# Performance work log

Hardware: AMD Instinct MI355X
Metric: run time of the kernel (lower is better)

Reference implementation:

```python
import jax, jax.numpy as jnp
import numpy as np

B, T, I, H, L, O = 256, 256, 512, 1024, 2, 5


def setup_inputs() -> dict:
    key = jax.random.key(0)
    ks = jax.random.split(key, 8)
    x = jax.random.normal(ks[0], (B, T, I), dtype=jnp.float32)
    hidden = jnp.zeros((L, 2, B, H), dtype=jnp.float32)  # [layer, (h,c), B, H]
    # per-layer stacked gate weights: [4(gates f,i,g,o), H, in+H]
    W0 = jax.random.normal(ks[1], (4, H, I + H), dtype=jnp.float32) * 0.01
    b0 = jnp.zeros((4, H), dtype=jnp.float32)
    W1 = jax.random.normal(ks[2], (4, H, H + H), dtype=jnp.float32) * 0.01
    b1 = jnp.zeros((4, H), dtype=jnp.float32)
    W_out = jax.random.normal(ks[3], (O, H), dtype=jnp.float32) * 0.01
    b_out = jnp.zeros((O,), dtype=jnp.float32)
    return {"x": x, "hidden": hidden, "W0": W0, "b0": b0,
            "W1": W1, "b1": b1, "W_out": W_out, "b_out": b_out}


def _lstm_cell(W, b):
    # W: [4, H, in+H], gates in order (f, i, g, o) matching the torch module
    def cell(carry, x_t):
        h, c = carry
        combined = jnp.concatenate([h, x_t], axis=1)        # [B, H+in]
        gates = jnp.einsum('bk,ghk->gbh', combined, W) + b[:, None, :]
        f = jax.nn.sigmoid(gates[0])
        i = jax.nn.sigmoid(gates[1])
        g = jnp.tanh(gates[2])
        o = jax.nn.sigmoid(gates[3])
        c_new = f * c + i * g
        h_new = o * jnp.tanh(c_new)
        return (h_new, c_new), h_new
    return cell


def reference(x, hidden, W0, b0, W1, b1, W_out, b_out):
    xs = jnp.swapaxes(x, 0, 1)  # [T, B, I]
    finals = []
    for layer, (W, b) in enumerate([(W0, b0), (W1, b1)]):
        h0, c0 = hidden[layer, 0], hidden[layer, 1]
        (hT, cT), ys = jax.lax.scan(_lstm_cell(W, b), (h0, c0), xs)
        xs = ys                      # feed this layer's h sequence to next layer
        finals.append(jnp.stack([hT, cT]))
    last_hidden = xs[-1]             # [B, H], last timestep of top layer
    output = last_hidden @ W_out.T + b_out
    return output, jnp.stack(finals)  # ([B,O], [L,2,B,H])
```

## Files before the change

### kernel.cpp

```cpp
#include <hip/hip_runtime.h>
#include <hip/hip_bf16.h>
#include <cstdint>
#include <cstddef>

#define Bdim 256
#define Tdim 256
#define Idim 512
#define Hdim 1024
#define Odim 5
#define BH (Bdim * Hdim)

using short8 = __attribute__((ext_vector_type(8))) short;
using f32x4  = __attribute__((ext_vector_type(4))) float;
typedef unsigned long long u64;

__device__ __forceinline__ short bf16_of(float f) {
  unsigned u = __builtin_bit_cast(unsigned, f);
  u += 0x7fffu + ((u >> 16) & 1u);
  return (short)(u >> 16);
}

__device__ __forceinline__ float sigmf(float x) {
  return 1.0f / (1.0f + __expf(-x));
}

__global__ __launch_bounds__(256) void k_init(const float* __restrict__ hidden,
    short* __restrict__ h0s0, short* __restrict__ h1s0) {
  int i = blockIdx.x * 256 + threadIdx.x;
  if (i < BH) {
    h0s0[i] = bf16_of(hidden[i]);
    h1s0[i] = bf16_of(hidden[2 * BH + i]);
  }
}

__device__ __forceinline__ void bar_arrive(unsigned* slots, unsigned val) {
  __syncthreads();
  if (threadIdx.x == 0)
    __hip_atomic_store(&slots[blockIdx.x], val, __ATOMIC_RELAXED,
                       __HIP_MEMORY_SCOPE_AGENT);
}

__device__ __forceinline__ void bar_poll(unsigned* slots, unsigned val) {
  if (threadIdx.x < 64) {
    unsigned* p = slots + threadIdx.x * 4;
    for (;;) {
      unsigned v0 = __hip_atomic_load(p + 0, __ATOMIC_RELAXED, __HIP_MEMORY_SCOPE_AGENT);
      unsigned v1 = __hip_atomic_load(p + 1, __ATOMIC_RELAXED, __HIP_MEMORY_SCOPE_AGENT);
      unsigned v2 = __hip_atomic_load(p + 2, __ATOMIC_RELAXED, __HIP_MEMORY_SCOPE_AGENT);
      unsigned v3 = __hip_atomic_load(p + 3, __ATOMIC_RELAXED, __HIP_MEMORY_SCOPE_AGENT);
      bool ok = (v0 >= val) & (v1 >= val) & (v2 >= val) & (v3 >= val);
      if (__all(ok)) break;
      __builtin_amdgcn_s_sleep(1);
    }
  }
}

#define GEMM_H(A0P, A1P, K0, NBLK)                                             \
  for (int blk = 0; blk < (NBLK); ++blk) {                                     \
    short8 Ar0[8], Ar1[8], Br0[8], Br1[8];                                     \
    const int kb = (K0) + blk * 256 + kl;                                      \
    _Pragma("unroll")                                                          \
    for (int u = 0; u < 8; ++u) {                                              \
      const int k = kb + u * 32;                                               \
      Ar0[u] = *(const short8*)((A0P) + k);                                    \
      Ar1[u] = *(const short8*)((A1P) + k);                                    \
      Br0[u] = *(const short8*)(lb0 + k);                                      \
      Br1[u] = *(const short8*)(lb1 + k);                                      \
    }                                                                          \
    _Pragma("unroll")                                                          \
    for (int u = 0; u < 8; ++u) {                                              \
      acc[0][0] = __builtin_amdgcn_mfma_f32_16x16x32_bf16(Ar0[u], Br0[u], acc[0][0], 0, 0, 0); \
      acc[1][0] = __builtin_amdgcn_mfma_f32_16x16x32_bf16(Ar1[u], Br0[u], acc[1][0], 0, 0, 0); \
      acc[0][1] = __builtin_amdgcn_mfma_f32_16x16x32_bf16(Ar0[u], Br1[u], acc[0][1], 0, 0, 0); \
      acc[1][1] = __builtin_amdgcn_mfma_f32_16x16x32_bf16(Ar1[u], Br1[u], acc[1][1], 0, 0, 0); \
    }                                                                          \
  }

#define GEMM_X(XF0, XF1)                                                       \
  for (int blk = 0; blk < 4; ++blk) {                                          \
    f32x4 U0[4][2], U1[4][2]; short8 Bx0[4], Bx1[4];                           \
    const int kb = Hdim + blk * 128 + kl;                                      \
    _Pragma("unroll")                                                          \
    for (int u = 0; u < 4; ++u) {                                              \
      const int k = kb + u * 32;                                               \
      U0[u][0] = *(const f32x4*)((XF0) + k);                                   \
      U0[u][1] = *(const f32x4*)((XF0) + k + 4);                               \
      U1[u][0] = *(const f32x4*)((XF1) + k);                                   \
      U1[u][1] = *(const f32x4*)((XF1) + k + 4);                               \
      Bx0[u] = *(const short8*)(lb0 + k);                                      \
      Bx1[u] = *(const short8*)(lb1 + k);                                      \
    }                                                                          \
    _Pragma("unroll")                                                          \
    for (int u = 0; u < 4; ++u) {                                              \
      short8 a0 = {bf16_of(U0[u][0][0]), bf16_of(U0[u][0][1]), bf16_of(U0[u][0][2]), bf16_of(U0[u][0][3]), \
                   bf16_of(U0[u][1][0]), bf16_of(U0[u][1][1]), bf16_of(U0[u][1][2]), bf16_of(U0[u][1][3])}; \
      short8 a1 = {bf16_of(U1[u][0][0]), bf16_of(U1[u][0][1]), bf16_of(U1[u][0][2]), bf16_of(U1[u][0][3]), \
                   bf16_of(U1[u][1][0]), bf16_of(U1[u][1][1]), bf16_of(U1[u][1][2]), bf16_of(U1[u][1][3])}; \
      acc[0][0] = __builtin_amdgcn_mfma_f32_16x16x32_bf16(a0, Bx0[u], acc[0][0], 0, 0, 0); \
      acc[1][0] = __builtin_amdgcn_mfma_f32_16x16x32_bf16(a1, Bx0[u], acc[1][0], 0, 0, 0); \
      acc[0][1] = __builtin_amdgcn_mfma_f32_16x16x32_bf16(a0, Bx1[u], acc[0][1], 0, 0, 0); \
      acc[1][1] = __builtin_amdgcn_mfma_f32_16x16x32_bf16(a1, Bx1[u], acc[1][1], 0, 0, 0); \
    }                                                                          \
  }

__global__ __launch_bounds__(512, 1) void k_persist(
    const float* __restrict__ W0, const float* __restrict__ b0v,
    const float* __restrict__ W1, const float* __restrict__ b1v,
    const float* __restrict__ hidden,
    const float* __restrict__ x,
    short* __restrict__ h0seq,
    short* __restrict__ h1seq,
    float* __restrict__ finals,
    unsigned* __restrict__ slots, int D) {
  extern __shared__ short lw[];
  const int tid  = threadIdx.x;
  const int wg   = blockIdx.x;
  const bool isL0 = (wg < 128);
  const int slot  = isL0 ? wg : wg - 128;
  const int hcol0 = slot * 8;
  const int K     = isL0 ? (Hdim + Idim) : (2 * Hdim);
  const int pitch = K + 8;
  const int layer = isL0 ? 0 : 1;
  const float* Wsrc = isL0 ? W0 : W1;
  const float* bsrc = isL0 ? b0v : b1v;

  for (int r = 0; r < 32; ++r) {
    const float* src = Wsrc + (size_t)((r >> 3) * Hdim + hcol0 + (r & 7)) * K;
    short* dst = lw + r * pitch;
    for (int k = tid; k < K; k += 512) dst[k] = bf16_of(src[k]);
  }

  const int lane = tid & 63;
  const int wv   = tid >> 6;
  const int col  = lane & 15;
  const int rg   = lane >> 4;
  const int kl   = rg * 8;
  const int row0 = wv * 32 + col;

  float biasv[2];
  #pragma unroll
  for (int n = 0; n < 2; ++n)
    biasv[n] = bsrc[(n * 2 + (col >= 8 ? 1 : 0)) * Hdim + hcol0 + (col & 7)];

  float creg[2][4], hfin[2][4];
  #pragma unroll
  for (int m = 0; m < 2; ++m)
    #pragma unroll
    for (int j = 0; j < 4; ++j) {
      int b = wv * 32 + m * 16 + rg * 4 + j;
      creg[m][j] = hidden[(layer * 2 + 1) * BH + b * Hdim + hcol0 + (col & 7)];
      hfin[m][j] = 0.f;
    }

  if (tid == 0)
    (void)__hip_atomic_load(slots, __ATOMIC_ACQUIRE, __HIP_MEMORY_SCOPE_AGENT);
  __syncthreads();

  const short* lb0 = lw + col * pitch;
  const short* lb1 = lw + (16 + col) * pitch;

  int i_cur = 0, i_prev = 0;
  for (int r = 0; r <= 256; ++r) {
    const bool active = isL0 ? (r < 256) : (r >= 1);
    const int t = isL0 ? r : r - 1;
    const int i_next = (i_cur + 1 == D) ? 0 : i_cur + 1;
    f32x4 acc[2][2] = {};

    if (active && isL0) {
      const float* xf0 = x + (size_t)(row0 * Tdim + t) * Idim - Hdim;
      const float* xf1 = x + (size_t)((row0 + 16) * Tdim + t) * Idim - Hdim;
      GEMM_X(xf0, xf1)
    }
    __builtin_amdgcn_sched_barrier(0);
    if (r > 0) {
      bar_poll(slots, (unsigned)r);
      if (tid == 0 && i_cur == 0)
        (void)__hip_atomic_load(slots, __ATOMIC_ACQUIRE, __HIP_MEMORY_SCOPE_AGENT);
      __syncthreads();
    }

    if (active) {
      const short* Ah = (isL0 ? h0seq + (size_t)i_cur * BH
                               : h1seq + (size_t)i_prev * BH) + row0 * Hdim;
      GEMM_H(Ah, Ah + 16 * Hdim, 0, 4)
      if (!isL0) {
        const short* Ax = h0seq + (size_t)i_cur * BH + row0 * Hdim - Hdim;
        GEMM_H(Ax, Ax + 16 * Hdim, Hdim, 4)
      }
      short* hout = isL0 ? h0seq + (size_t)i_next * BH
                         : h1seq + (size_t)i_cur * BH;
      #pragma unroll
      for (int m = 0; m < 2; ++m) {
        #pragma unroll
        for (int j = 0; j < 4; ++j) {
          float fi  = acc[m][0][j] + biasv[0];
          float go  = acc[m][1][j] + biasv[1];
          float iv_ = __shfl_xor(fi, 8, 64);
          float ov_ = __shfl_xor(go, 8, 64);
          float fv = sigmf(fi), iv = sigmf(iv_);
          float gv = tanhf(go), ov = sigmf(ov_);
          float cn = fv * creg[m][j] + iv * gv;
          creg[m][j] = cn;
          float hn = ov * tanhf(cn);
          hfin[m][j] = hn;
          unsigned hv = (unsigned)(unsigned short)bf16_of(hn);
          unsigned p1 = hv | ((unsigned)__shfl_xor((int)hv, 1, 64) << 16);
          u64 p2 = (u64)p1 | ((u64)(unsigned)__shfl_xor((int)p1, 2, 64) << 32);
          if ((col & 3) == 0 && col < 8) {
            int b = wv * 32 + m * 16 + rg * 4 + j;
            __hip_atomic_store((u64*)(hout + b * Hdim + hcol0 + col), p2,
                               __ATOMIC_RELAXED, __HIP_MEMORY_SCOPE_AGENT);
          }
        }
      }
    }
    if (r < 256) bar_arrive(slots, (unsigned)(r + 1));
    i_prev = i_cur; i_cur = i_next;
  }

  if (col < 8) {
    #pragma unroll
    for (int m = 0; m < 2; ++m)
      #pragma unroll
      for (int j = 0; j < 4; ++j) {
        int b = wv * 32 + m * 16 + rg * 4 + j;
        finals[(layer * 2 + 0) * BH + b * Hdim + hcol0 + col] = hfin[m][j];
        finals[(layer * 2 + 1) * BH + b * Hdim + hcol0 + col] = creg[m][j];
      }
  }
}

__global__ __launch_bounds__(256) void k_outproj(const float* __restrict__ h1f,
    const float* __restrict__ Wout, const float* __restrict__ bout,
    float* __restrict__ out) {
  int b = blockIdx.x;
  int tid = threadIdx.x;
  float hv[4];
  #pragma unroll
  for (int j = 0; j < 4; ++j) hv[j] = h1f[b * Hdim + tid + j * 256];
  __shared__ float red[Odim][4];
  #pragma unroll
  for (int o = 0; o < Odim; ++o) {
    float p = 0.f;
    #pragma unroll
    for (int j = 0; j < 4; ++j) p += hv[j] * Wout[o * Hdim + tid + j * 256];
    #pragma unroll
    for (int s = 32; s > 0; s >>= 1) p += __shfl_down(p, s, 64);
    if ((tid & 63) == 0) red[o][tid >> 6] = p;
  }
  __syncthreads();
  if (tid < Odim)
    out[b * Odim + tid] = red[tid][0] + red[tid][1] + red[tid][2] + red[tid][3] + bout[tid];
}

extern "C" void kernel_launch(void* const* d_in, const int* in_sizes, int n_in,
                              void* d_out, int out_size, void* d_ws, size_t ws_size,
                              hipStream_t stream) {
  const float* x      = (const float*)d_in[0];
  const float* hidden = (const float*)d_in[1];
  const float* W0     = (const float*)d_in[2];
  const float* b0     = (const float*)d_in[3];
  const float* W1     = (const float*)d_in[4];
  const float* b1     = (const float*)d_in[5];
  const float* Wout   = (const float*)d_in[6];
  const float* bout   = (const float*)d_in[7];
  float* out = (float*)d_out;
  float* finals = out + Bdim * Odim;

  char* ws = (char*)d_ws;
  size_t off = 0;
  auto alloc = [&](size_t bytes) {
    void* p = ws + off;
    off += (bytes + 255) & ~(size_t)255;
    return p;
  };
  unsigned* slots = (unsigned*)alloc(256 * sizeof(unsigned));
  const size_t seqSlotBytes = (size_t)BH * 2;
  size_t avail = (ws_size > off) ? (ws_size - off - 512) : 0;
  int D = (int)(avail / (2 * seqSlotBytes));
  if (D > 257) D = 257;
  if (D < 2) D = 2;
  short* h0seq = (short*)alloc((size_t)D * seqSlotBytes);
  short* h1seq = (short*)alloc((size_t)D * seqSlotBytes);

  k_init<<<BH / 256, 256, 0, stream>>>(hidden, h0seq, h1seq);
  hipMemsetAsync(slots, 0, 256 * sizeof(unsigned), stream);

  const int ldsBytes = 32 * (2 * Hdim + 8) * 2;
  hipFuncSetAttribute((const void*)k_persist,
                      hipFuncAttributeMaxDynamicSharedMemorySize, ldsBytes);
  void* args[] = {(void*)&W0, (void*)&b0, (void*)&W1, (void*)&b1,
                  (void*)&hidden, (void*)&x,
                  (void*)&h0seq, (void*)&h1seq,
                  (void*)&finals, (void*)&slots, (void*)&D};
  hipLaunchCooperativeKernel((const void*)k_persist, dim3(256), dim3(512),
                             args, ldsBytes, stream);

  k_outproj<<<Bdim, 256, 0, stream>>>(finals + 2 * BH, Wout, bout, out);
}
```

Before: 8.661 ms.

## Replace global per-step barrier with per-layer counters and decoupled layer pipelining

Swaps the all-256-workgroup slot barrier for 16 padded atomic counters, eight per layer, that workgroups increment. Layer 0 now waits only on its own layer's step count, plus a bounded-lead check against layer 1 so ring buffer slots are not overwritten. Layer 1 waits on layer 0's step r+1 and its own step r, so the two layers can drift apart instead of running in lockstep. The intent is to cut barrier polling cost and let the two layers overlap more freely. In exchange the minimum ring depth rises to 8 and there is more contention from atomic adds on shared counters.

```diff
diff --git a/kernel.cpp b/kernel.cpp
--- a/kernel.cpp
+++ b/kernel.cpp
@@ -33,22 +33,25 @@
   }
 }
 
-__device__ __forceinline__ void bar_arrive(unsigned* slots, unsigned val) {
+__device__ __forceinline__ void ctr_arrive(unsigned* ctr, int c) {
+  __builtin_amdgcn_sched_barrier(0);
   __syncthreads();
   if (threadIdx.x == 0)
-    __hip_atomic_store(&slots[blockIdx.x], val, __ATOMIC_RELAXED,
-                       __HIP_MEMORY_SCOPE_AGENT);
-}
-
-__device__ __forceinline__ void bar_poll(unsigned* slots, unsigned val) {
+    __hip_atomic_fetch_add(&ctr[c * 32], 1u, __ATOMIC_RELAXED,
+                           __HIP_MEMORY_SCOPE_AGENT);
+}
+
+__device__ __forceinline__ void ctr_poll2(unsigned* ctr, unsigned tg0, unsigned tg1) {
   if (threadIdx.x < 64) {
-    unsigned* p = slots + threadIdx.x * 4;
+    const int lane = threadIdx.x;
+    const unsigned tgt = (lane < 8) ? tg0 : (lane < 16 ? tg1 : 0u);
+    unsigned* p = ctr + (lane < 16 ? lane : 0) * 32;
     for (;;) {
-      unsigned v0 = __hip_atomic_load(p + 0, __ATOMIC_RELAXED, __HIP_MEMORY_SCOPE_AGENT);
-      unsigned v1 = __hip_atomic_load(p + 1, __ATOMIC_RELAXED, __HIP_MEMORY_SCOPE_AGENT);
-      unsigned v2 = __hip_atomic_load(p + 2, __ATOMIC_RELAXED, __HIP_MEMORY_SCOPE_AGENT);
-      unsigned v3 = __hip_atomic_load(p + 3, __ATOMIC_RELAXED, __HIP_MEMORY_SCOPE_AGENT);
-      bool ok = (v0 >= val) & (v1 >= val) & (v2 >= val) & (v3 >= val);
+      bool ok = true;
+      if (tgt) {
+        unsigned v = __hip_atomic_load(p, __ATOMIC_RELAXED, __HIP_MEMORY_SCOPE_AGENT);
+        ok = (v >= tgt);
+      }
       if (__all(ok)) break;
       __builtin_amdgcn_s_sleep(1);
     }
@@ -111,7 +114,7 @@
     short* __restrict__ h0seq,
     short* __restrict__ h1seq,
     float* __restrict__ finals,
-    unsigned* __restrict__ slots, int D) {
+    unsigned* __restrict__ ctr, int D) {
   extern __shared__ short lw[];
   const int tid  = threadIdx.x;
   const int wg   = blockIdx.x;
@@ -121,6 +124,8 @@
   const int K     = isL0 ? (Hdim + Idim) : (2 * Hdim);
   const int pitch = K + 8;
   const int layer = isL0 ? 0 : 1;
+  const int myc   = layer * 8 + (wg & 7);
+  const int lead  = D - 4;
   const float* Wsrc = isL0 ? W0 : W1;
   const float* bsrc = isL0 ? b0v : b1v;
 
@@ -153,69 +158,69 @@
     }
 
   if (tid == 0)
-    (void)__hip_atomic_load(slots, __ATOMIC_ACQUIRE, __HIP_MEMORY_SCOPE_AGENT);
+    (void)__hip_atomic_load(ctr, __ATOMIC_ACQUIRE, __HIP_MEMORY_SCOPE_AGENT);
   __syncthreads();
 
   const short* lb0 = lw + col * pitch;
   const short* lb1 = lw + (16 + col) * pitch;
 
-  int i_cur = 0, i_prev = 0;
-  for (int r = 0; r <= 256; ++r) {
-    const bool active = isL0 ? (r < 256) : (r >= 1);
-    const int t = isL0 ? r : r - 1;
+  int i_cur = 0;
+  for (int r = 0; r < 256; ++r) {
     const int i_next = (i_cur + 1 == D) ? 0 : i_cur + 1;
     f32x4 acc[2][2] = {};
-
-    if (active && isL0) {
-      const float* xf0 = x + (size_t)(row0 * Tdim + t) * Idim - Hdim;
-      const float* xf1 = x + (size_t)((row0 + 16) * Tdim + t) * Idim - Hdim;
+    short* hout;
+
+    if (isL0) {
+      const float* xf0 = x + (size_t)(row0 * Tdim + r) * Idim - Hdim;
+      const float* xf1 = x + (size_t)((row0 + 16) * Tdim + r) * Idim - Hdim;
       GEMM_X(xf0, xf1)
+      __builtin_amdgcn_sched_barrier(0);
+      unsigned tg1 = (r > lead) ? 16u * (unsigned)(r - lead) : 0u;
+      if (r > 0 || tg1) ctr_poll2(ctr, 16u * (unsigned)r, tg1);
+      if (tid == 0 && D < 257 && r >= D - 1)
+        (void)__hip_atomic_load(ctr, __ATOMIC_ACQUIRE, __HIP_MEMORY_SCOPE_AGENT);
+      __syncthreads();
+      const short* Ah = h0seq + (size_t)i_cur * BH + row0 * Hdim;
+      GEMM_H(Ah, Ah + 16 * Hdim, 0, 4)
+      hout = h0seq + (size_t)i_next * BH;
+    } else {
+      ctr_poll2(ctr, 16u * (unsigned)(r + 1), 16u * (unsigned)r);
+      if (tid == 0 && D < 257 && r >= D - 1)
+        (void)__hip_atomic_load(ctr, __ATOMIC_ACQUIRE, __HIP_MEMORY_SCOPE_AGENT);
+      __syncthreads();
+      const short* Ax = h0seq + (size_t)i_next * BH + row0 * Hdim - Hdim;
+      GEMM_H(Ax, Ax + 16 * Hdim, Hdim, 4)
+      const short* Ah = h1seq + (size_t)i_cur * BH + row0 * Hdim;
+      GEMM_H(Ah, Ah + 16 * Hdim, 0, 4)
+      hout = h1seq + (size_t)i_next * BH;
     }
-    __builtin_amdgcn_sched_barrier(0);
-    if (r > 0) {
-      bar_poll(slots, (unsigned)r);
-      if (tid == 0 && i_cur == 0)
-        (void)__hip_atomic_load(slots, __ATOMIC_ACQUIRE, __HIP_MEMORY_SCOPE_AGENT);
-      __syncthreads();
-    }
-
-    if (active) {
-      const short* Ah = (isL0 ? h0seq + (size_t)i_cur * BH
-                               : h1seq + (size_t)i_prev * BH) + row0 * Hdim;
-      GEMM_H(Ah, Ah + 16 * Hdim, 0, 4)
-      if (!isL0) {
-        const short* Ax = h0seq + (size_t)i_cur * BH + row0 * Hdim - Hdim;
-        GEMM_H(Ax, Ax + 16 * Hdim, Hdim, 4)
-      }
-      short* hout = isL0 ? h0seq + (size_t)i_next * BH
-                         : h1seq + (size_t)i_cur * BH;
+
+    #pragma unroll
+    for (int m = 0; m < 2; ++m) {
       #pragma unroll
-      for (int m = 0; m < 2; ++m) {
-        #pragma unroll
-        for (int j = 0; j < 4; ++j) {
-          float fi  = acc[m][0][j] + biasv[0];
-          float go  = acc[m][1][j] + biasv[1];
-          float iv_ = __shfl_xor(fi, 8, 64);
-          float ov_ = __shfl_xor(go, 8, 64);
-          float fv = sigmf(fi), iv = sigmf(iv_);
-          float gv = tanhf(go), ov = sigmf(ov_);
-          float cn = fv * creg[m][j] + iv * gv;
-          creg[m][j] = cn;
-          float hn = ov * tanhf(cn);
-          hfin[m][j] = hn;
-          unsigned hv = (unsigned)(unsigned short)bf16_of(hn);
-          unsigned p1 = hv | ((unsigned)__shfl_xor((int)hv, 1, 64) << 16);
-          u64 p2 = (u64)p1 | ((u64)(unsigned)__shfl_xor((int)p1, 2, 64) << 32);
-          if ((col & 3) == 0 && col < 8) {
-            int b = wv * 32 + m * 16 + rg * 4 + j;
-            __hip_atomic_store((u64*)(hout + b * Hdim + hcol0 + col), p2,
-                               __ATOMIC_RELAXED, __HIP_MEMORY_SCOPE_AGENT);
-          }
+      for (int j = 0; j < 4; ++j) {
+        float fi  = acc[m][0][j] + biasv[0];
+        float go  = acc[m][1][j] + biasv[1];
+        float iv_ = __shfl_xor(fi, 8, 64);
+        float ov_ = __shfl_xor(go, 8, 64);
+        float fv = sigmf(fi), iv = sigmf(iv_);
+        float gv = tanhf(go), ov = sigmf(ov_);
+        float cn = fv * creg[m][j] + iv * gv;
+        creg[m][j] = cn;
+        float hn = ov * tanhf(cn);
+        hfin[m][j] = hn;
+        unsigned hv = (unsigned)(unsigned short)bf16_of(hn);
+        unsigned p1 = hv | ((unsigned)__shfl_xor((int)hv, 1, 64) << 16);
+        u64 p2 = (u64)p1 | ((u64)(unsigned)__shfl_xor((int)p1, 2, 64) << 32);
+        if ((col & 3) == 0 && col < 8) {
+          int b = wv * 32 + m * 16 + rg * 4 + j;
+          __hip_atomic_store((u64*)(hout + b * Hdim + hcol0 + col), p2,
+                             __ATOMIC_RELAXED, __HIP_MEMORY_SCOPE_AGENT);
         }
       }
     }
-    if (r < 256) bar_arrive(slots, (unsigned)(r + 1));
-    i_prev = i_cur; i_cur = i_next;
+    ctr_arrive(ctr, myc);
+    i_cur = i_next;
   }
 
   if (col < 8) {
@@ -274,17 +279,17 @@
     off += (bytes + 255) & ~(size_t)255;
     return p;
   };
-  unsigned* slots = (unsigned*)alloc(256 * sizeof(unsigned));
+  unsigned* ctr = (unsigned*)alloc(16 * 32 * sizeof(unsigned));
   const size_t seqSlotBytes = (size_t)BH * 2;
   size_t avail = (ws_size > off) ? (ws_size - off - 512) : 0;
   int D = (int)(avail / (2 * seqSlotBytes));
   if (D > 257) D = 257;
-  if (D < 2) D = 2;
+  if (D < 8) D = 8;
   short* h0seq = (short*)alloc((size_t)D * seqSlotBytes);
   short* h1seq = (short*)alloc((size_t)D * seqSlotBytes);
 
   k_init<<<BH / 256, 256, 0, stream>>>(hidden, h0seq, h1seq);
-  hipMemsetAsync(slots, 0, 256 * sizeof(unsigned), stream);
+  hipMemsetAsync(ctr, 0, 16 * 32 * sizeof(unsigned), stream);
 
   const int ldsBytes = 32 * (2 * Hdim + 8) * 2;
   hipFuncSetAttribute((const void*)k_persist,
@@ -292,7 +297,7 @@
   void* args[] = {(void*)&W0, (void*)&b0, (void*)&W1, (void*)&b1,
                   (void*)&hidden, (void*)&x,
                   (void*)&h0seq, (void*)&h1seq,
-                  (void*)&finals, (void*)&slots, (void*)&D};
+                  (void*)&finals, (void*)&ctr, (void*)&D};
   hipLaunchCooperativeKernel((const void*)k_persist, dim3(256), dim3(512),
                              args, ldsBytes, stream);
 
```

Measured after the change: 8.249 ms. 1.05x faster.
